# Performance work log

Measured on AMD Instinct MI355X. Metric: run time of the kernel, lower is better.

## Reference

```python
import jax, jax.numpy as jnp
import numpy as np

H = 16
D_MODEL = 1024
D_K = D_MODEL // H
B, S = 4, 2048


def setup_inputs() -> dict:
    key = jax.random.key(0)
    ks = jax.random.split(key, 12)
    scale = 1.0 / np.sqrt(D_MODEL)
    inp = {
        "q": jax.random.normal(ks[0], (B, S, D_MODEL), dtype=jnp.float32),
        "k": jax.random.normal(ks[1], (B, S, D_MODEL), dtype=jnp.float32),
        "v": jax.random.normal(ks[2], (B, S, D_MODEL), dtype=jnp.float32),
        # torch nn.Linear weights: shape (out, in), y = x @ W.T + b
        "Wq": jax.random.uniform(ks[3], (D_MODEL, D_MODEL), minval=-scale, maxval=scale),
        "bq": jax.random.uniform(ks[4], (D_MODEL,), minval=-scale, maxval=scale),
        "Wk": jax.random.uniform(ks[5], (D_MODEL, D_MODEL), minval=-scale, maxval=scale),
        "bk": jax.random.uniform(ks[6], (D_MODEL,), minval=-scale, maxval=scale),
        "Wv": jax.random.uniform(ks[7], (D_MODEL, D_MODEL), minval=-scale, maxval=scale),
        "bv": jax.random.uniform(ks[8], (D_MODEL,), minval=-scale, maxval=scale),
        "Wo": jax.random.uniform(ks[9], (D_MODEL, D_MODEL), minval=-scale, maxval=scale),
        "bo": jax.random.uniform(ks[10], (D_MODEL,), minval=-scale, maxval=scale),
        "ln_g": jnp.ones((D_MODEL,), dtype=jnp.float32),
        "ln_b": jnp.zeros((D_MODEL,), dtype=jnp.float32),
    }
    return inp


def _layernorm(x, g, b, eps=1e-5):
    mu = jnp.mean(x, axis=-1, keepdims=True)
    var = jnp.var(x, axis=-1, keepdims=True)
    return (x - mu) * jax.lax.rsqrt(var + eps) * g + b


def reference(q, k, v, Wq, bq, Wk, bk, Wv, bv, Wo, bo, ln_g, ln_b):
    nb = q.shape[0]
    # projections, split heads -> (B, H, S, d_k)
    def proj(x, W, b):
        y = x @ W.T + b
        return y.reshape(nb, -1, H, D_K).transpose(0, 2, 1, 3)

    Q = proj(q, Wq, bq)
    K = proj(k, Wk, bk)
    V = proj(v, Wv, bv)

    scores = jnp.einsum("bhqd,bhkd->bhqk", Q, K) / jnp.sqrt(jnp.float32(D_K))
    p_attn = jax.nn.softmax(scores, axis=-1)
    x = jnp.einsum("bhqk,bhkd->bhqd", p_attn, V)
    x = x.transpose(0, 2, 1, 3).reshape(nb, -1, H * D_K)
    out = _layernorm(x @ Wo.T + bo + q, ln_g, ln_b)
    return out
```

## Files before the change

kernel.cpp:

```cpp
#include <hip/hip_runtime.h>

#define DM 1024
#define NH 16
#define DK 64
#define SEQ 2048
#define BATCH 4
#define M_TOT (BATCH * SEQ)

typedef short s16x8 __attribute__((ext_vector_type(8)));
typedef float f32x4 __attribute__((ext_vector_type(4)));
typedef unsigned int u32x4 __attribute__((ext_vector_type(4)));

#define MFMA16(a, b, c) __builtin_amdgcn_mfma_f32_16x16x32_bf16((a), (b), (c), 0, 0, 0)

#define QSCALE 0.1803368801111244f

__device__ __forceinline__ float bf2f(unsigned short u) {
    return __uint_as_float(((unsigned int)u) << 16);
}
__device__ __forceinline__ unsigned short f2bf(float f) {
    unsigned int u = __float_as_uint(f);
    u += 0x7FFFu + ((u >> 16) & 1u);
    return (unsigned short)(u >> 16);
}
__device__ __forceinline__ unsigned int pack_bf2(unsigned int lo, unsigned int hi) {
    return ((lo + 0x8000u) >> 16) | ((hi + 0x8000u) & 0xFFFF0000u);
}
__device__ __forceinline__ unsigned int pack_bf2_trunc(float lo, float hi) {
    return __builtin_amdgcn_perm(__float_as_uint(hi), __float_as_uint(lo), 0x07060302u);
}
__device__ __forceinline__ s16x8 load_cvt8(const float* p) {
    u32x4 x0 = *reinterpret_cast<const u32x4*>(p);
    u32x4 x1 = *reinterpret_cast<const u32x4*>(p + 4);
    union { s16x8 v; unsigned int u[4]; } r;
    r.u[0] = pack_bf2(x0[0], x0[1]);
    r.u[1] = pack_bf2(x0[2], x0[3]);
    r.u[2] = pack_bf2(x1[0], x1[1]);
    r.u[3] = pack_bf2(x1[2], x1[3]);
    return r.v;
}

__device__ __forceinline__ void ld_lds16(const unsigned short* g, unsigned short* lds_base) {
    __builtin_amdgcn_global_load_lds(
        (const __attribute__((address_space(1))) unsigned int*)g,
        (__attribute__((address_space(3))) unsigned int*)lds_base,
        16, 0, 0);
}

__global__ __launch_bounds__(256) void cvt_bf16_kernel(
    const float* __restrict__ src, unsigned short* __restrict__ dst, int n)
{
    const int i = (blockIdx.x * 256 + threadIdx.x) * 8;
    if (i >= n) return;
    *reinterpret_cast<s16x8*>(dst + i) = load_cvt8(src + i);
}

__global__ __launch_bounds__(256) void cvt3_kernel(
    const float* __restrict__ s0, const float* __restrict__ s1,
    const float* __restrict__ s2, unsigned short* __restrict__ dst)
{
    const float* src = blockIdx.z == 0 ? s0 : blockIdx.z == 1 ? s1 : s2;
    const long off = (long)blockIdx.z * ((long)M_TOT * DM);
    const int i = (blockIdx.x * 256 + threadIdx.x) * 8;
    *reinterpret_cast<s16x8*>(dst + off + i) = load_cvt8(src + i);
}

__global__ __launch_bounds__(256) void cvt_w_kernel(
    const float* __restrict__ w0, const float* __restrict__ w1,
    const float* __restrict__ w2, const float* __restrict__ w3,
    unsigned short* __restrict__ dst)
{
    const float* src = blockIdx.y == 0 ? w0 : blockIdx.y == 1 ? w1
                     : blockIdx.y == 2 ? w2 : w3;
    const long off = (long)blockIdx.y * ((long)DM * DM);
    const int i = (blockIdx.x * 256 + threadIdx.x) * 8;
    *reinterpret_cast<s16x8*>(dst + off + i) = load_cvt8(src + i);
}

__device__ __forceinline__ void gemm_body(
    const unsigned short* __restrict__ Ab,
    const unsigned short* __restrict__ Wb,
    const float* __restrict__ bias,
    unsigned short* __restrict__ Y,
    const int mode, const float scale)
{
    const int tid  = threadIdx.x;
    const int lane = tid & 63;
    const int wave = tid >> 6;
    const int c16  = lane & 15;
    const int quad = lane >> 4;

    const int flat  = blockIdx.y * gridDim.x + blockIdx.x;
    const int xcd   = flat & 7;
    const int w     = flat >> 3;
    const int m_blk = xcd * 8 + (w & 7);
    const int n_blk = w >> 3;
    const int m0 = m_blk * 128;
    const int n0 = n_blk * 128;

    const int wm = (wave >> 1) * 64;
    const int wn = (wave & 1) * 64;

    __shared__ __align__(16) unsigned short As[128 * 32];
    __shared__ __align__(16) unsigned short Bs[128 * 32];

    f32x4 acc[4][4];
    #pragma unroll
    for (int tm = 0; tm < 4; ++tm)
        #pragma unroll
        for (int tn = 0; tn < 4; ++tn) acc[tm][tn] = (f32x4){0.f, 0.f, 0.f, 0.f};

    int srow[2], sch[2];
    #pragma unroll
    for (int c = 0; c < 2; ++c) {
        const int s = c * 256 + wave * 64 + lane;
        srow[c] = s >> 2;
        sch[c]  = s & 3;
    }

    for (int k0 = 0; k0 < DM; k0 += 32) {
        #pragma unroll
        for (int c = 0; c < 2; ++c) {
            unsigned short* abase = As + (c * 256 + wave * 64) * 8;
            unsigned short* bbase = Bs + (c * 256 + wave * 64) * 8;
            ld_lds16(Ab + (long)(m0 + srow[c]) * DM + k0 + sch[c] * 8, abase);
            ld_lds16(Wb + (long)(n0 + srow[c]) * DM + k0 + sch[c] * 8, bbase);
        }
        __syncthreads();

        s16x8 a[4], b[4];
        #pragma unroll
        for (int tm = 0; tm < 4; ++tm)
            a[tm] = *reinterpret_cast<const s16x8*>(As + (wm + tm * 16 + c16) * 32 + quad * 8);
        #pragma unroll
        for (int tn = 0; tn < 4; ++tn)
            b[tn] = *reinterpret_cast<const s16x8*>(Bs + (wn + tn * 16 + c16) * 32 + quad * 8);
        #pragma unroll
        for (int tm = 0; tm < 4; ++tm)
            #pragma unroll
            for (int tn = 0; tn < 4; ++tn)
                acc[tm][tn] = MFMA16(a[tm], b[tn], acc[tm][tn]);
        __syncthreads();
    }

    #pragma unroll
    for (int tn = 0; tn < 4; ++tn) {
        const int col = n0 + wn + tn * 16 + c16;
        const float bv = bias[col];
        const int h = col >> 6, d = col & 63;
        #pragma unroll
        for (int tm = 0; tm < 4; ++tm) {
            #pragma unroll
            for (int r = 0; r < 4; ++r) {
                const int m = m0 + wm + tm * 16 + quad * 4 + r;
                const int b_ = m >> 11;
                const int s  = m & 2047;
                const float v = (acc[tm][tn][r] + bv) * scale;
                long idx;
                if (mode == 0)      idx = (((long)(b_ * NH + h) * SEQ + s) * DK) + d;
                else if (mode == 1) idx = (((long)(b_ * NH + h) * DK + d) * SEQ) + s;
                else                idx = (long)m * DM + col;
                Y[idx] = f2bf(v);
            }
        }
    }
}

__global__ __launch_bounds__(256) void gemm_kernel(
    const unsigned short* __restrict__ Ab,
    const unsigned short* __restrict__ Wb,
    const float* __restrict__ bias,
    unsigned short* __restrict__ Y,
    const int mode, const float scale)
{
    gemm_body(Ab, Wb, bias, Y, mode, scale);
}

__global__ __launch_bounds__(256) void gemm3_kernel(
    const unsigned short* __restrict__ A3,
    const unsigned short* __restrict__ W3,
    const float* __restrict__ bq, const float* __restrict__ bk,
    const float* __restrict__ bv,
    unsigned short* __restrict__ Y3)
{
    const int z = blockIdx.z;
    const long NE = (long)M_TOT * DM;
    const long WEl = (long)DM * DM;
    const unsigned short* Ab = A3 + (long)z * NE;
    const unsigned short* Wb = W3 + (long)z * WEl;
    const float* bias = z == 0 ? bq : z == 1 ? bk : bv;
    unsigned short* Y = Y3 + (long)z * NE;
    const int mode = (z == 2) ? 1 : 0;
    const float scale = (z == 0) ? QSCALE : 1.0f;
    gemm_body(Ab, Wb, bias, Y, mode, scale);
}

__global__ __launch_bounds__(256, 4) void attn_kernel(
    const unsigned short* __restrict__ Qh,
    const unsigned short* __restrict__ Kh,
    const unsigned short* __restrict__ Vt,
    unsigned short* __restrict__ Xo)
{
    const int lane = threadIdx.x & 63;
    const int wave = threadIdx.x >> 6;
    const int c16  = lane & 15;
    const int quad = lane >> 4;
    const int bh = blockIdx.x;
    const int b_ = bh >> 4, h = bh & 15;
    const int m0 = blockIdx.y * 128 + wave * 32;

    __shared__ __align__(16) unsigned short Ks[2 * 64 * 64];
    __shared__ __align__(16) unsigned short Vs[2 * 64 * 64];

    const unsigned short* Kbh = Kh + (long)bh * SEQ * DK;
    const unsigned short* Vbh = Vt + (long)bh * DK * SEQ;

    s16x8 bQ[2][2];
    #pragma unroll
    for (int qt = 0; qt < 2; ++qt) {
        const unsigned short* qb = Qh + ((long)bh * SEQ + m0 + qt * 16 + c16) * DK + quad * 8;
        bQ[qt][0] = *reinterpret_cast<const s16x8*>(qb);
        bQ[qt][1] = *reinterpret_cast<const s16x8*>(qb + 32);
    }

    union { s16x8 v; unsigned int u[4]; } onesu;
    onesu.u[0] = 0x3F803F80u; onesu.u[1] = 0x3F803F80u;
    onesu.u[2] = 0x3F803F80u; onesu.u[3] = 0x3F803F80u;
    const s16x8 onesA = onesu.v;

    f32x4 o[2][4];
    f32x4 lacc[2];
    #pragma unroll
    for (int qt = 0; qt < 2; ++qt) {
        #pragma unroll
        for (int c = 0; c < 4; ++c) o[qt][c] = (f32x4){0.f, 0.f, 0.f, 0.f};
        lacc[qt] = (f32x4){0.f, 0.f, 0.f, 0.f};
    }

    int st_src[4], st_x[4], st_isK[4];
    #pragma unroll
    for (int j = 0; j < 4; ++j) {
        const int c = wave * 4 + j;
        const int s = (c & 7) * 64 + lane;
        const int m = s >> 3;
        st_isK[j] = (c < 8);
        st_x[j] = (s & 7) ^ (m & 7);
        st_src[j] = st_isK[j]
            ? ( (((m >> 4) & 1) << 5) | (((m >> 2) & 3) << 3) | (((m >> 5) & 1) << 2) | (m & 3) )
            : m;
    }

    auto stage = [&](int buf, int n0) {
        #pragma unroll
        for (int j = 0; j < 4; ++j) {
            const int c = wave * 4 + j;
            if (st_isK[j])
                ld_lds16(Kbh + (n0 + st_src[j]) * DK + st_x[j] * 8,
                         &Ks[buf * 4096 + (c & 7) * 512]);
            else
                ld_lds16(Vbh + (long)st_src[j] * SEQ + n0 + st_x[j] * 8,
                         &Vs[buf * 4096 + (c & 7) * 512]);
        }
    };

    stage(0, 0);
    __syncthreads();

    for (int it = 0; it < SEQ / 64; ++it) {
        const int cur = it & 1;
        if (it + 1 < SEQ / 64) stage(cur ^ 1, (it + 1) * 64);

        const unsigned short* Kb = Ks + cur * 4096;
        const unsigned short* Vb = Vs + cur * 4096;

        f32x4 st[2][4];
        __builtin_amdgcn_s_setprio(1);
        #pragma unroll
        for (int t = 0; t < 4; ++t) {
            const int n = t * 16 + c16;
            const int sw = n & 7;
            s16x8 a0 = *reinterpret_cast<const s16x8*>(&Kb[n * 64 + ((quad ^ sw) * 8)]);
            s16x8 a1 = *reinterpret_cast<const s16x8*>(&Kb[n * 64 + (((quad + 4) ^ sw) * 8)]);
            #pragma unroll
            for (int qt = 0; qt < 2; ++qt) {
                f32x4 s = (f32x4){0.f, 0.f, 0.f, 0.f};
                s = MFMA16(a0, bQ[qt][0], s);
                s = MFMA16(a1, bQ[qt][1], s);
                st[qt][t] = s;
            }
        }
        __builtin_amdgcn_s_setprio(0);

        s16x8 bP[2][2];
        #pragma unroll
        for (int qt = 0; qt < 2; ++qt) {
            #pragma unroll
            for (int t = 0; t < 4; ++t)
                #pragma unroll
                for (int r = 0; r < 4; ++r)
                    st[qt][t][r] = exp2f(st[qt][t][r]);

            #pragma unroll
            for (int hh = 0; hh < 2; ++hh) {
                union { s16x8 v; unsigned int u[4]; } f;
                f.u[0] = pack_bf2_trunc(st[qt][hh][0],     st[qt][hh][1]);
                f.u[1] = pack_bf2_trunc(st[qt][hh][2],     st[qt][hh][3]);
                f.u[2] = pack_bf2_trunc(st[qt][hh + 2][0], st[qt][hh + 2][1]);
                f.u[3] = pack_bf2_trunc(st[qt][hh + 2][2], st[qt][hh + 2][3]);
                bP[qt][hh] = f.v;
            }
        }

        __builtin_amdgcn_s_setprio(1);
        #pragma unroll
        for (int qt = 0; qt < 2; ++qt) {
            lacc[qt] = MFMA16(onesA, bP[qt][0], lacc[qt]);
            lacc[qt] = MFMA16(onesA, bP[qt][1], lacc[qt]);
        }
        #pragma unroll
        for (int cc = 0; cc < 4; ++cc) {
            const int d = cc * 16 + c16;
            const int sw = d & 7;
            s16x8 a0 = *reinterpret_cast<const s16x8*>(&Vb[d * 64 + ((quad ^ sw) * 8)]);
            s16x8 a1 = *reinterpret_cast<const s16x8*>(&Vb[d * 64 + (((quad + 4) ^ sw) * 8)]);
            #pragma unroll
            for (int qt = 0; qt < 2; ++qt) {
                o[qt][cc] = MFMA16(a0, bP[qt][0], o[qt][cc]);
                o[qt][cc] = MFMA16(a1, bP[qt][1], o[qt][cc]);
            }
        }
        __builtin_amdgcn_s_setprio(0);
        __syncthreads();
    }

    #pragma unroll
    for (int qt = 0; qt < 2; ++qt) {
        const float inv = 1.f / lacc[qt][0];
        unsigned short* orow = Xo + ((long)b_ * SEQ + m0 + qt * 16 + c16) * DM + h * DK;
        #pragma unroll
        for (int c = 0; c < 4; ++c) {
            uint2 w;
            w.x = pack_bf2(__float_as_uint(o[qt][c][0] * inv), __float_as_uint(o[qt][c][1] * inv));
            w.y = pack_bf2(__float_as_uint(o[qt][c][2] * inv), __float_as_uint(o[qt][c][3] * inv));
            *reinterpret_cast<uint2*>(orow + c * 16 + quad * 4) = w;
        }
    }
}

__global__ __launch_bounds__(256) void ln_kernel(
    const unsigned short* __restrict__ Xlin,
    const float* __restrict__ qres,
    const float* __restrict__ g,
    const float* __restrict__ bb,
    float* __restrict__ out)
{
    const int row = blockIdx.x;
    const int tid = threadIdx.x;
    const int c0 = tid * 4;
    const int lane = tid & 63, wave = tid >> 6;

    __shared__ float ssum[4], ssq[4];

    uint2 xb = *reinterpret_cast<const uint2*>(Xlin + (long)row * DM + c0);
    float4 qv = *reinterpret_cast<const float4*>(qres + (long)row * DM + c0);
    float v[4];
    v[0] = bf2f((unsigned short)(xb.x & 0xFFFF)) + qv.x;
    v[1] = bf2f((unsigned short)(xb.x >> 16))    + qv.y;
    v[2] = bf2f((unsigned short)(xb.y & 0xFFFF)) + qv.z;
    v[3] = bf2f((unsigned short)(xb.y >> 16))    + qv.w;

    float s = v[0] + v[1] + v[2] + v[3];
    float q2 = v[0]*v[0] + v[1]*v[1] + v[2]*v[2] + v[3]*v[3];
    #pragma unroll
    for (int d = 1; d < 64; d <<= 1) {
        s  += __shfl_xor(s, d, 64);
        q2 += __shfl_xor(q2, d, 64);
    }
    if (lane == 0) { ssum[wave] = s; ssq[wave] = q2; }
    __syncthreads();
    const float ts = ssum[0] + ssum[1] + ssum[2] + ssum[3];
    const float tq = ssq[0] + ssq[1] + ssq[2] + ssq[3];
    const float mu = ts * (1.f / 1024.f);
    const float var = tq * (1.f / 1024.f) - mu * mu;
    const float rstd = rsqrtf(var + 1e-5f);

    float4 gv = *reinterpret_cast<const float4*>(g + c0);
    float4 bv = *reinterpret_cast<const float4*>(bb + c0);
    float4 o;
    o.x = (v[0] - mu) * rstd * gv.x + bv.x;
    o.y = (v[1] - mu) * rstd * gv.y + bv.y;
    o.z = (v[2] - mu) * rstd * gv.z + bv.z;
    o.w = (v[3] - mu) * rstd * gv.w + bv.w;
    *reinterpret_cast<float4*>(out + (long)row * DM + c0) = o;
}

extern "C" void kernel_launch(void* const* d_in, const int* in_sizes, int n_in,
                              void* d_out, int out_size, void* d_ws, size_t ws_size,
                              hipStream_t stream) {
    const float* q   = (const float*)d_in[0];
    const float* k   = (const float*)d_in[1];
    const float* v   = (const float*)d_in[2];
    const float* Wq  = (const float*)d_in[3];
    const float* bq  = (const float*)d_in[4];
    const float* Wk  = (const float*)d_in[5];
    const float* bk  = (const float*)d_in[6];
    const float* Wv  = (const float*)d_in[7];
    const float* bvv = (const float*)d_in[8];
    const float* Wo  = (const float*)d_in[9];
    const float* bo  = (const float*)d_in[10];
    const float* lng = (const float*)d_in[11];
    const float* lnb = (const float*)d_in[12];

    unsigned short* ws = (unsigned short*)d_ws;
    const long WE = (long)DM * DM;
    const long NE = (long)M_TOT * DM;

    dim3 blk(256);
    const int cvtW = (int)(WE / 2048);
    const int cvtX = (int)(NE / 2048);
    dim3 ggemm(M_TOT / 128, DM / 128);

    const size_t need_batched = (size_t)(4 * WE + 6 * NE) * sizeof(unsigned short);

    if (ws_size >= need_batched) {
        unsigned short* Wqb = ws;
        unsigned short* Wob = Wqb + 3 * WE;
        unsigned short* A3  = Wqb + 4 * WE;
        unsigned short* O3  = A3 + 3 * NE;
        unsigned short* Xo   = A3;
        unsigned short* Xlin = A3 + NE;

        cvt_w_kernel<<<dim3(cvtW, 4), blk, 0, stream>>>(Wq, Wk, Wv, Wo, Wqb);
        cvt3_kernel<<<dim3(cvtX, 1, 3), blk, 0, stream>>>(q, k, v, A3);
        gemm3_kernel<<<dim3(M_TOT / 128, DM / 128, 3), blk, 0, stream>>>(
            A3, Wqb, bq, bk, bvv, O3);
        attn_kernel<<<dim3(BATCH * NH, SEQ / 128), blk, 0, stream>>>(
            O3, O3 + NE, O3 + 2 * NE, Xo);
        gemm_kernel<<<ggemm, blk, 0, stream>>>(Xo, Wob, bo, Xlin, 2, 1.0f);
        ln_kernel<<<dim3(M_TOT), blk, 0, stream>>>(Xlin, q, lng, lnb, (float*)d_out);
    } else {
        unsigned short* Wqb = ws;
        unsigned short* Wkb = Wqb + WE;
        unsigned short* Wvb = Wkb + WE;
        unsigned short* Wob = Wvb + WE;
        unsigned short* U1  = Wob + WE;
        unsigned short* U2  = U1 + NE;
        unsigned short* U3  = U2 + NE;
        unsigned short* U4  = U3 + NE;

        cvt_w_kernel<<<dim3(cvtW, 4), blk, 0, stream>>>(Wq, Wk, Wv, Wo, Wqb);
        cvt_bf16_kernel<<<cvtX, blk, 0, stream>>>(q, U1, (int)NE);
        gemm_kernel<<<ggemm, blk, 0, stream>>>(U1, Wqb, bq, U2, 0, QSCALE);
        cvt_bf16_kernel<<<cvtX, blk, 0, stream>>>(k, U1, (int)NE);
        gemm_kernel<<<ggemm, blk, 0, stream>>>(U1, Wkb, bk, U3, 0, 1.0f);
        cvt_bf16_kernel<<<cvtX, blk, 0, stream>>>(v, U1, (int)NE);
        gemm_kernel<<<ggemm, blk, 0, stream>>>(U1, Wvb, bvv, U4, 1, 1.0f);
        attn_kernel<<<dim3(BATCH * NH, SEQ / 128), blk, 0, stream>>>(U2, U3, U4, U1);
        gemm_kernel<<<ggemm, blk, 0, stream>>>(U1, Wob, bo, U2, 2, 1.0f);
        ln_kernel<<<dim3(M_TOT), blk, 0, stream>>>(U2, q, lng, lnb, (float*)d_out);
    }
}
```

Before: 382.5 us.

## Double GEMM K-tile to 64 with XOR-swizzled LDS and merge conversion kernels

The shared GEMM body now stages a 64-wide K slice per iteration instead of 32. This halves the number of barrier pairs and doubles the MFMA work between syncs. An XOR swizzle on the LDS column index is meant to avoid bank conflicts on the wider rows. Separately, the weight and activation fp32-to-bf16 conversion launches are merged into one kernel to save a launch. LDS use doubles, which may reduce occupancy.

```diff
diff --git a/kernel.cpp b/kernel.cpp
--- a/kernel.cpp
+++ b/kernel.cpp
@@ -55,13 +55,32 @@
     *reinterpret_cast<s16x8*>(dst + i) = load_cvt8(src + i);
 }
 
-__global__ __launch_bounds__(256) void cvt3_kernel(
-    const float* __restrict__ s0, const float* __restrict__ s1,
-    const float* __restrict__ s2, unsigned short* __restrict__ dst)
-{
-    const float* src = blockIdx.z == 0 ? s0 : blockIdx.z == 1 ? s1 : s2;
-    const long off = (long)blockIdx.z * ((long)M_TOT * DM);
-    const int i = (blockIdx.x * 256 + threadIdx.x) * 8;
+__global__ __launch_bounds__(256) void cvt_all_kernel(
+    const float* __restrict__ w0, const float* __restrict__ w1,
+    const float* __restrict__ w2, const float* __restrict__ w3,
+    const float* __restrict__ a0, const float* __restrict__ a1,
+    const float* __restrict__ a2, unsigned short* __restrict__ dst)
+{
+    const long WE = (long)DM * DM;
+    const long NE = (long)M_TOT * DM;
+    const int id = blockIdx.x;
+    const float* src;
+    long off;
+    int i;
+    if (id < 2048) {
+        const int wsel = id >> 9;
+        const int blk  = id & 511;
+        src = wsel == 0 ? w0 : wsel == 1 ? w1 : wsel == 2 ? w2 : w3;
+        off = (long)wsel * WE;
+        i = blk * 2048 + threadIdx.x * 8;
+    } else {
+        const int id2  = id - 2048;
+        const int asel = id2 >> 12;
+        const int blk  = id2 & 4095;
+        src = asel == 0 ? a0 : asel == 1 ? a1 : a2;
+        off = 4 * WE + (long)asel * NE;
+        i = blk * 2048 + threadIdx.x * 8;
+    }
     *reinterpret_cast<s16x8*>(dst + off + i) = load_cvt8(src + i);
 }
 
@@ -101,8 +120,8 @@
     const int wm = (wave >> 1) * 64;
     const int wn = (wave & 1) * 64;
 
-    __shared__ __align__(16) unsigned short As[128 * 32];
-    __shared__ __align__(16) unsigned short Bs[128 * 32];
+    __shared__ __align__(16) unsigned short As[128 * 64];
+    __shared__ __align__(16) unsigned short Bs[128 * 64];
 
     f32x4 acc[4][4];
     #pragma unroll
@@ -110,36 +129,42 @@
         #pragma unroll
         for (int tn = 0; tn < 4; ++tn) acc[tm][tn] = (f32x4){0.f, 0.f, 0.f, 0.f};
 
-    int srow[2], sch[2];
-    #pragma unroll
-    for (int c = 0; c < 2; ++c) {
+    int srow[4], scol[4];
+    #pragma unroll
+    for (int c = 0; c < 4; ++c) {
         const int s = c * 256 + wave * 64 + lane;
-        srow[c] = s >> 2;
-        sch[c]  = s & 3;
-    }
-
-    for (int k0 = 0; k0 < DM; k0 += 32) {
-        #pragma unroll
-        for (int c = 0; c < 2; ++c) {
-            unsigned short* abase = As + (c * 256 + wave * 64) * 8;
-            unsigned short* bbase = Bs + (c * 256 + wave * 64) * 8;
-            ld_lds16(Ab + (long)(m0 + srow[c]) * DM + k0 + sch[c] * 8, abase);
-            ld_lds16(Wb + (long)(n0 + srow[c]) * DM + k0 + sch[c] * 8, bbase);
+        srow[c] = s >> 3;
+        scol[c] = ((s & 7) ^ (srow[c] & 7)) * 8;
+    }
+
+    const int xa = ((quad ^ (c16 & 7)) * 8);
+
+    for (int k0 = 0; k0 < DM; k0 += 64) {
+        #pragma unroll
+        for (int c = 0; c < 4; ++c) {
+            ld_lds16(Ab + (long)(m0 + srow[c]) * DM + k0 + scol[c],
+                     As + (c * 256 + wave * 64) * 8);
+            ld_lds16(Wb + (long)(n0 + srow[c]) * DM + k0 + scol[c],
+                     Bs + (c * 256 + wave * 64) * 8);
         }
         __syncthreads();
 
-        s16x8 a[4], b[4];
-        #pragma unroll
-        for (int tm = 0; tm < 4; ++tm)
-            a[tm] = *reinterpret_cast<const s16x8*>(As + (wm + tm * 16 + c16) * 32 + quad * 8);
-        #pragma unroll
-        for (int tn = 0; tn < 4; ++tn)
-            b[tn] = *reinterpret_cast<const s16x8*>(Bs + (wn + tn * 16 + c16) * 32 + quad * 8);
-        #pragma unroll
-        for (int tm = 0; tm < 4; ++tm)
+        #pragma unroll
+        for (int kk = 0; kk < 2; ++kk) {
+            const int xo = xa ^ (kk << 5);
+            s16x8 a[4], b[4];
+            #pragma unroll
+            for (int tm = 0; tm < 4; ++tm)
+                a[tm] = *reinterpret_cast<const s16x8*>(As + (wm + tm * 16 + c16) * 64 + xo);
             #pragma unroll
             for (int tn = 0; tn < 4; ++tn)
-                acc[tm][tn] = MFMA16(a[tm], b[tn], acc[tm][tn]);
+                b[tn] = *reinterpret_cast<const s16x8*>(Bs + (wn + tn * 16 + c16) * 64 + xo);
+            #pragma unroll
+            for (int tm = 0; tm < 4; ++tm)
+                #pragma unroll
+                for (int tn = 0; tn < 4; ++tn)
+                    acc[tm][tn] = MFMA16(a[tm], b[tn], acc[tm][tn]);
+        }
         __syncthreads();
     }
 
@@ -430,8 +455,8 @@
         unsigned short* Xo   = A3;
         unsigned short* Xlin = A3 + NE;
 
-        cvt_w_kernel<<<dim3(cvtW, 4), blk, 0, stream>>>(Wq, Wk, Wv, Wo, Wqb);
-        cvt3_kernel<<<dim3(cvtX, 1, 3), blk, 0, stream>>>(q, k, v, A3);
+        cvt_all_kernel<<<dim3(2048 + 3 * 4096), blk, 0, stream>>>(
+            Wq, Wk, Wv, Wo, q, k, v, ws);
         gemm3_kernel<<<dim3(M_TOT / 128, DM / 128, 3), blk, 0, stream>>>(
             A3, Wqb, bq, bk, bvv, O3);
         attn_kernel<<<dim3(BATCH * NH, SEQ / 128), blk, 0, stream>>>(
```

Result: faster. 374.2 us (-2.1%).
